# Kernel tuning notes

Measured on AMD Instinct MI355X. Metric: run time of the kernel, lower is better.

Reference implementation:

```python
import jax, jax.numpy as jnp
import numpy as np
from jax import lax

N = 8192
D = 128
CHUNK = 128  # rows of adj processed per scan step; bounds the [CHUNK, N, D] masked intermediate


def setup_inputs() -> dict:
    key = jax.random.key(0)
    k1, k2 = jax.random.split(key)
    x = jax.random.normal(k1, (N, D), dtype=jnp.float32)
    adj = jax.random.randint(k2, (N, N), 0, 2, dtype=jnp.int32)
    return {"x": x, "adj": adj}


def reference(x, adj):
    # For each node i: max over features of its neighbors (adj[i] nonzero),
    # or zeros if it has no neighbors. Equivalent to a masked row-max.
    n, d = x.shape
    neg = jnp.finfo(x.dtype).min
    adj_chunks = adj.reshape(n // CHUNK, CHUNK, n)

    def step(carry, a):  # a: [CHUNK, n]
        mask = a != 0
        # masked: [CHUNK, n, d] — neighbors keep x, non-neighbors get -inf-like
        masked = jnp.where(mask[:, :, None], x[None, :, :], neg)
        m = jnp.max(masked, axis=1)                      # [CHUNK, d]
        has_nbr = jnp.any(mask, axis=1)                  # [CHUNK]
        out = jnp.where(has_nbr[:, None], m, jnp.zeros((), x.dtype))
        return carry, out

    _, out = lax.scan(step, None, adj_chunks)
    return out.reshape(n, d)
```

## Files before the change

kernel.cpp:

```cpp
#include <hip/hip_runtime.h>
#include <cfloat>
#include <cstdint>

#define NN 8192
#define DD 128
#define WPR 256
#define TOPK 32

__device__ __forceinline__ uint32_t f2s(float f) {
  uint32_t u = __float_as_uint(f);
  return (u & 0x80000000u) ? ~u : (u | 0x80000000u);
}
__device__ __forceinline__ float s2f(uint32_t s) {
  return (s & 0x80000000u) ? __uint_as_float(s & 0x7fffffffu)
                           : __uint_as_float(~s);
}
__device__ __forceinline__ unsigned long long shfl_down_u64(unsigned long long v, int off) {
  unsigned lo = __shfl_down((unsigned)(v & 0xffffffffull), off, 64);
  unsigned hi = __shfl_down((unsigned)(v >> 32), off, 64);
  return ((unsigned long long)hi << 32) | (unsigned long long)lo;
}

__global__ __launch_bounds__(256) void prep_kernel(
    const float* __restrict__ x, const int* __restrict__ adj,
    uint32_t* __restrict__ bits, int* __restrict__ has_nbr,
    float* __restrict__ tkv, int* __restrict__ tki) {
  const int b = blockIdx.x;
  const int t = threadIdx.x;

  __shared__ unsigned long long red[4];
  __shared__ unsigned long long bcast;
  __shared__ int anyflag;

  if (b >= DD) {
    const int row = b - DD;
    const uint4* src = ((const uint4*)(adj + (size_t)row * NN)) + (size_t)t * 8;
    uint32_t w = 0;
#pragma unroll
    for (int c = 0; c < 8; ++c) {
      uint4 v = src[c];
      w |= (v.x ? 1u : 0u) << (4 * c + 0);
      w |= (v.y ? 1u : 0u) << (4 * c + 1);
      w |= (v.z ? 1u : 0u) << (4 * c + 2);
      w |= (v.w ? 1u : 0u) << (4 * c + 3);
    }
    bits[(size_t)row * WPR + t] = w;
    if (t == 0) anyflag = 0;
    __syncthreads();
    if (w) anyflag = 1;
    __syncthreads();
    if (t == 0) has_nbr[row] = anyflag;
  } else {
    const int d = b;
    float vals[32];
#pragma unroll
    for (int e = 0; e < 32; ++e) {
      int j = t * 32 + e;
      vals[e] = x[(size_t)j * DD + d];
    }
    unsigned long long prev = ~0ull;
    for (int k = 0; k < TOPK; ++k) {
      unsigned long long best = 0ull;
#pragma unroll
      for (int e = 0; e < 32; ++e) {
        int j = t * 32 + e;
        unsigned long long key =
            ((unsigned long long)f2s(vals[e]) << 32) | (unsigned)j;
        if (key < prev && key > best) best = key;
      }
      for (int off = 32; off; off >>= 1) {
        unsigned long long o = shfl_down_u64(best, off);
        if (o > best) best = o;
      }
      const int lane = t & 63, wv = t >> 6;
      if (lane == 0) red[wv] = best;
      __syncthreads();
      if (t == 0) {
        unsigned long long m = red[0];
        for (int i = 1; i < 4; ++i) if (red[i] > m) m = red[i];
        bcast = m;
        uint32_t s = (uint32_t)(m >> 32);
        uint32_t j = (uint32_t)(m & 0xffffffffu);
        tkv[k * DD + d] = s2f(s);
        tki[k * DD + d] = (int)j;
      }
      __syncthreads();
      prev = bcast;
    }
  }
}

__global__ __launch_bounds__(256) void probe_kernel(
    const float* __restrict__ x, const uint32_t* __restrict__ bits,
    const int* __restrict__ has_nbr, const float* __restrict__ tkv,
    const int* __restrict__ tki, float* __restrict__ out) {
  const int t = threadIdx.x;
  const int row = blockIdx.x * 2 + (t >> 7);
  const int d = t & 127;
  const uint32_t* rb = bits + (size_t)row * WPR;

  float res = 0.0f;
  bool done = false;
  for (int k = 0; k < TOPK; ++k) {
    int idx = tki[k * DD + d];
    float val = tkv[k * DD + d];
    uint32_t w = rb[idx >> 5];
    bool hit = (w >> (idx & 31)) & 1u;
    if (!done && hit) { res = val; done = true; }
    if (__all((int)done)) break;
  }
  if (__any((int)(!done))) {
    if (!done && has_nbr[row]) {
      float m = -FLT_MAX;
      for (int wd = 0; wd < WPR; ++wd) {
        uint32_t bm = rb[wd];
        while (bm) {
          int j = wd * 32 + __ffs(bm) - 1;
          bm &= bm - 1;
          m = fmaxf(m, x[(size_t)j * DD + d]);
        }
      }
      res = m;
    }
  }
  out[(size_t)row * DD + d] = res;
}

extern "C" void kernel_launch(void* const* d_in, const int* in_sizes, int n_in,
                              void* d_out, int out_size, void* d_ws, size_t ws_size,
                              hipStream_t stream) {
  const float* x = (const float*)d_in[0];
  const int* adj = (const int*)d_in[1];
  float* out = (float*)d_out;

  uint32_t* bits = (uint32_t*)d_ws;
  int* has_nbr = (int*)((char*)d_ws + (size_t)NN * WPR * 4);
  float* tkv = (float*)((char*)has_nbr + (size_t)NN * 4);
  int* tki = (int*)((char*)tkv + (size_t)TOPK * DD * 4);

  prep_kernel<<<NN + DD, 256, 0, stream>>>(x, adj, bits, has_nbr, tkv, tki);
  probe_kernel<<<NN / 2, 256, 0, stream>>>(x, bits, has_nbr, tkv, tki, out);
}
```

Measured before the change: 370.7 us.

## Coalesce adjacency bitpacking with wave ballots and pack top-k into float2

The adjacency packing now has each thread load strided uint4 elements so that a wave reads contiguous memory, and builds 64-bit masks with __ballot instead of having every thread read 128 contiguous bytes. This produces a permuted bit layout, so the probe kernel remaps neighbor indices to match. Top-k values and indices are stored together as a float2, and the keys are precomputed once outside the selection loop. The intent is to cut the uncoalesced-load cost of reading the 256MB adjacency matrix, which dominates runtime. The cost is extra index arithmetic and a more complex bit layout.

```diff
diff --git a/kernel.cpp b/kernel.cpp
--- a/kernel.cpp
+++ b/kernel.cpp
@@ -4,7 +4,7 @@
 
 #define NN 8192
 #define DD 128
-#define WPR 256
+#define W64PR 128
 #define TOPK 32
 
 __device__ __forceinline__ uint32_t f2s(float f) {
@@ -15,18 +15,16 @@
   return (s & 0x80000000u) ? __uint_as_float(s & 0x7fffffffu)
                            : __uint_as_float(~s);
 }
-__device__ __forceinline__ unsigned long long shfl_down_u64(unsigned long long v, int off) {
-  unsigned lo = __shfl_down((unsigned)(v & 0xffffffffull), off, 64);
-  unsigned hi = __shfl_down((unsigned)(v >> 32), off, 64);
-  return ((unsigned long long)hi << 32) | (unsigned long long)lo;
-}
+
 
 __global__ __launch_bounds__(256) void prep_kernel(
     const float* __restrict__ x, const int* __restrict__ adj,
-    uint32_t* __restrict__ bits, int* __restrict__ has_nbr,
-    float* __restrict__ tkv, int* __restrict__ tki) {
+    unsigned long long* __restrict__ bits, int* __restrict__ has_nbr,
+    float2* __restrict__ tk) {
   const int b = blockIdx.x;
   const int t = threadIdx.x;
+  const int lane = t & 63;
+  const int wv = t >> 6;
 
   __shared__ unsigned long long red[4];
   __shared__ unsigned long long bcast;
@@ -34,55 +32,58 @@
 
   if (b >= DD) {
     const int row = b - DD;
-    const uint4* src = ((const uint4*)(adj + (size_t)row * NN)) + (size_t)t * 8;
-    uint32_t w = 0;
+    const uint4* src = (const uint4*)(adj + (size_t)row * NN);
+    unsigned long long* dst = bits + (size_t)row * W64PR;
+    if (t == 0) anyflag = 0;
+    __syncthreads();
+    unsigned long long any = 0;
 #pragma unroll
     for (int c = 0; c < 8; ++c) {
-      uint4 v = src[c];
-      w |= (v.x ? 1u : 0u) << (4 * c + 0);
-      w |= (v.y ? 1u : 0u) << (4 * c + 1);
-      w |= (v.z ? 1u : 0u) << (4 * c + 2);
-      w |= (v.w ? 1u : 0u) << (4 * c + 3);
+      uint4 v = src[c * 256 + t];
+      unsigned long long b0 = __ballot(v.x != 0);
+      unsigned long long b1 = __ballot(v.y != 0);
+      unsigned long long b2 = __ballot(v.z != 0);
+      unsigned long long b3 = __ballot(v.w != 0);
+      any |= (b0 | b1 | b2 | b3);
+      if (lane == 0) {
+        ulonglong2* p = (ulonglong2*)(dst + (c * 16 + wv * 4));
+        ulonglong2 q0; q0.x = b0; q0.y = b1;
+        ulonglong2 q1; q1.x = b2; q1.y = b3;
+        p[0] = q0;
+        p[1] = q1;
+      }
     }
-    bits[(size_t)row * WPR + t] = w;
-    if (t == 0) anyflag = 0;
-    __syncthreads();
-    if (w) anyflag = 1;
+    if (lane == 0 && any) anyflag = 1;
     __syncthreads();
     if (t == 0) has_nbr[row] = anyflag;
   } else {
     const int d = b;
-    float vals[32];
+    unsigned long long key[32];
 #pragma unroll
     for (int e = 0; e < 32; ++e) {
       int j = t * 32 + e;
-      vals[e] = x[(size_t)j * DD + d];
+      key[e] = ((unsigned long long)f2s(x[(size_t)j * DD + d]) << 32) | (unsigned)j;
     }
     unsigned long long prev = ~0ull;
     for (int k = 0; k < TOPK; ++k) {
       unsigned long long best = 0ull;
 #pragma unroll
-      for (int e = 0; e < 32; ++e) {
-        int j = t * 32 + e;
-        unsigned long long key =
-            ((unsigned long long)f2s(vals[e]) << 32) | (unsigned)j;
-        if (key < prev && key > best) best = key;
-      }
+      for (int e = 0; e < 32; ++e)
+        if (key[e] < prev && key[e] > best) best = key[e];
       for (int off = 32; off; off >>= 1) {
-        unsigned long long o = shfl_down_u64(best, off);
+        unsigned long long o = __shfl_down(best, off, 64);
         if (o > best) best = o;
       }
-      const int lane = t & 63, wv = t >> 6;
       if (lane == 0) red[wv] = best;
       __syncthreads();
       if (t == 0) {
         unsigned long long m = red[0];
         for (int i = 1; i < 4; ++i) if (red[i] > m) m = red[i];
         bcast = m;
-        uint32_t s = (uint32_t)(m >> 32);
-        uint32_t j = (uint32_t)(m & 0xffffffffu);
-        tkv[k * DD + d] = s2f(s);
-        tki[k * DD + d] = (int)j;
+        float2 kv;
+        kv.x = s2f((uint32_t)(m >> 32));
+        kv.y = __int_as_float((int)(uint32_t)(m & 0xffffffffu));
+        tk[k * DD + d] = kv;
       }
       __syncthreads();
       prev = bcast;
@@ -91,32 +92,37 @@
 }
 
 __global__ __launch_bounds__(256) void probe_kernel(
-    const float* __restrict__ x, const uint32_t* __restrict__ bits,
-    const int* __restrict__ has_nbr, const float* __restrict__ tkv,
-    const int* __restrict__ tki, float* __restrict__ out) {
+    const float* __restrict__ x, const unsigned long long* __restrict__ bits,
+    const int* __restrict__ has_nbr, const float2* __restrict__ tk,
+    float* __restrict__ out) {
   const int t = threadIdx.x;
   const int row = blockIdx.x * 2 + (t >> 7);
   const int d = t & 127;
-  const uint32_t* rb = bits + (size_t)row * WPR;
+  const uint32_t* rb32 = (const uint32_t*)(bits + (size_t)row * W64PR);
 
   float res = 0.0f;
   bool done = false;
   for (int k = 0; k < TOPK; ++k) {
-    int idx = tki[k * DD + d];
-    float val = tkv[k * DD + d];
-    uint32_t w = rb[idx >> 5];
-    bool hit = (w >> (idx & 31)) & 1u;
-    if (!done && hit) { res = val; done = true; }
+    float2 kv = tk[k * DD + d];
+    int idx = __float_as_int(kv.y);
+    int i64 = ((idx >> 10) << 4) | (((idx >> 8) & 3) << 2) | (idx & 3);
+    int l = (idx >> 2) & 63;
+    uint32_t w = rb32[i64 * 2 + (l >> 5)];
+    bool hit = (w >> (l & 31)) & 1u;
+    if (!done && hit) { res = kv.x; done = true; }
     if (__all((int)done)) break;
   }
   if (__any((int)(!done))) {
     if (!done && has_nbr[row]) {
       float m = -FLT_MAX;
-      for (int wd = 0; wd < WPR; ++wd) {
-        uint32_t bm = rb[wd];
+      const unsigned long long* rb64 = bits + (size_t)row * W64PR;
+      for (int i = 0; i < W64PR; ++i) {
+        unsigned long long bm = rb64[i];
+        int base = ((i >> 4) << 10) + (((i >> 2) & 3) << 8) + (i & 3);
         while (bm) {
-          int j = wd * 32 + __ffs(bm) - 1;
+          int l2 = __ffsll((unsigned long long)bm) - 1;
           bm &= bm - 1;
+          int j = base + 4 * l2;
           m = fmaxf(m, x[(size_t)j * DD + d]);
         }
       }
@@ -133,11 +139,10 @@
   const int* adj = (const int*)d_in[1];
   float* out = (float*)d_out;
 
-  uint32_t* bits = (uint32_t*)d_ws;
-  int* has_nbr = (int*)((char*)d_ws + (size_t)NN * WPR * 4);
-  float* tkv = (float*)((char*)has_nbr + (size_t)NN * 4);
-  int* tki = (int*)((char*)tkv + (size_t)TOPK * DD * 4);
+  unsigned long long* bits = (unsigned long long*)d_ws;
+  int* has_nbr = (int*)((char*)d_ws + (size_t)NN * W64PR * 8);
+  float2* tk = (float2*)((char*)has_nbr + (size_t)NN * 4);
 
-  prep_kernel<<<NN + DD, 256, 0, stream>>>(x, adj, bits, has_nbr, tkv, tki);
-  probe_kernel<<<NN / 2, 256, 0, stream>>>(x, bits, has_nbr, tkv, tki, out);
+  prep_kernel<<<NN + DD, 256, 0, stream>>>(x, adj, bits, has_nbr, tk);
+  probe_kernel<<<NN / 2, 256, 0, stream>>>(x, bits, has_nbr, tk, out);
 }
```

Result: no change. 374.8 us (+1.1%).
